# Performance work log

Hardware: AMD Instinct MI355X
Metric: run time of the kernel (lower is better)

Reference implementation:

```python
import jax, jax.numpy as jnp
import numpy as np

N, F_IN, HID, H1, E = 50000, 512, 128, 4, 800000
NEG_SLOPE = 0.2

def setup_inputs() -> dict:
    key = jax.random.key(0)
    ks = jax.random.split(key, 10)
    s = lambda fan: 1.0 / np.sqrt(fan)
    x = jax.random.normal(ks[0], (N, F_IN), jnp.float32)
    edge_index = jax.random.randint(ks[1], (2, E), 0, N, jnp.int32)
    W1 = jax.random.normal(ks[2], (F_IN, H1 * HID), jnp.float32) * s(F_IN)
    a_src1 = jax.random.normal(ks[3], (H1, HID), jnp.float32) * s(HID)
    a_dst1 = jax.random.normal(ks[4], (H1, HID), jnp.float32) * s(HID)
    b1 = jnp.zeros((H1 * HID,), jnp.float32)
    W2 = jax.random.normal(ks[5], (H1 * HID, HID), jnp.float32) * s(H1 * HID)
    a_src2 = jax.random.normal(ks[6], (1, HID), jnp.float32) * s(HID)
    a_dst2 = jax.random.normal(ks[7], (1, HID), jnp.float32) * s(HID)
    b2 = jnp.zeros((HID,), jnp.float32)
    return {"x": x, "edge_index": edge_index, "W1": W1, "a_src1": a_src1,
            "a_dst1": a_dst1, "b1": b1, "W2": W2, "a_src2": a_src2,
            "a_dst2": a_dst2, "b2": b2}

def _gat(x, src, dst, W, a_src, a_dst, b, n):
    H, C = a_src.shape
    h = (x @ W).reshape(-1, H, C)                      # [N, H, C]
    # per-edge attention logits: alpha_src[src] + alpha_dst[dst]
    e = jax.nn.leaky_relu((h * a_src).sum(-1)[src] + (h * a_dst).sum(-1)[dst],
                          NEG_SLOPE)                   # [E', H]
    # segment softmax over destination node
    m = jax.ops.segment_max(e, dst, num_segments=n)
    p = jnp.exp(e - m[dst])
    denom = jax.ops.segment_sum(p, dst, num_segments=n)
    alpha = p / (denom[dst] + 1e-16)
    # weighted scatter-add aggregation
    out = jax.ops.segment_sum(h[src] * alpha[:, :, None], dst, num_segments=n)
    return out.reshape(-1, H * C) + b

def reference(x, edge_index, W1, a_src1, a_dst1, b1, W2, a_src2, a_dst2, b2):
    loops = jnp.arange(N, dtype=edge_index.dtype)      # add_self_loops=True
    src = jnp.concatenate([edge_index[0], loops])
    dst = jnp.concatenate([edge_index[1], loops])
    h = jax.nn.elu(_gat(x, src, dst, W1, a_src1, a_dst1, b1, N))
    return _gat(h, src, dst, W2, a_src2, a_dst2, b2, N)
```

## Files before the change

kernel.cpp:

```cpp
#include <hip/hip_runtime.h>
#include <hip/hip_bf16.h>
#include <math.h>

#define NEG_SLOPE 0.2f

constexpr int N_NODES = 50000;
constexpr int F_IN    = 512;
constexpr int HID     = 128;
constexpr int H1      = 4;
constexpr int E_EDGES = 800000;
constexpr int E_TOT   = E_EDGES + N_NODES;

typedef __attribute__((ext_vector_type(8))) short short8;
typedef __attribute__((ext_vector_type(4))) float floatx4;
typedef __attribute__((ext_vector_type(8))) unsigned short ushort8v;
typedef __attribute__((ext_vector_type(4))) unsigned short ushort4v;
typedef __attribute__((ext_vector_type(2))) unsigned short ushort2v;

__device__ __forceinline__ unsigned short f2bf(float f) {
  union { float f; unsigned int u; } v; v.f = f;
  unsigned int u = v.u + 0x7FFFu + ((v.u >> 16) & 1u);
  return (unsigned short)(u >> 16);
}
__device__ __forceinline__ float bf2f(unsigned short b) {
  union { unsigned int u; float f; } v; v.u = ((unsigned int)b) << 16; return v.f;
}

__device__ __forceinline__ void store_val(float* p, float v) { *p = v; }
__device__ __forceinline__ void store_val(unsigned short* p, float v) { *p = f2bf(v); }

template <int CPT>
__device__ __forceinline__ void load_cvt(const unsigned short* p, float* v) {
  if constexpr (CPT == 8) {
    ushort8v u = *(const ushort8v*)p;
#pragma unroll
    for (int c = 0; c < 8; ++c) v[c] = bf2f(u[c]);
  } else if constexpr (CPT == 4) {
    ushort4v u = *(const ushort4v*)p;
#pragma unroll
    for (int c = 0; c < 4; ++c) v[c] = bf2f(u[c]);
  } else {
    ushort2v u = *(const ushort2v*)p;
#pragma unroll
    for (int c = 0; c < 2; ++c) v[c] = bf2f(u[c]);
  }
}
template <int CPT>
__device__ __forceinline__ void load_cvt(const float* p, float* v) {
#pragma unroll
  for (int c = 0; c < CPT; c += 4) *(float4*)(v + c) = *(const float4*)(p + c);
}

template <int CPT>
__device__ __forceinline__ void store_vec(unsigned short* p, const float* v) {
  if constexpr (CPT == 8) {
    ushort8v o;
#pragma unroll
    for (int c = 0; c < 8; ++c) o[c] = f2bf(v[c]);
    *(ushort8v*)p = o;
  } else if constexpr (CPT == 4) {
    ushort4v o;
#pragma unroll
    for (int c = 0; c < 4; ++c) o[c] = f2bf(v[c]);
    *(ushort4v*)p = o;
  } else {
    ushort2v o;
#pragma unroll
    for (int c = 0; c < 2; ++c) o[c] = f2bf(v[c]);
    *(ushort2v*)p = o;
  }
}
template <int CPT>
__device__ __forceinline__ void store_vec(float* p, const float* v) {
#pragma unroll
  for (int c = 0; c < CPT; c += 4) *(float4*)(p + c) = *(const float4*)(v + c);
}

__device__ __forceinline__ void async_load16(const void* g, void* lds) {
  __builtin_amdgcn_global_load_lds(
      (const __attribute__((address_space(1))) unsigned int*)g,
      (__attribute__((address_space(3))) unsigned int*)lds, 16, 0, 0);
}

__global__ void zero_int_kernel(int* p, int n) {
  int i = blockIdx.x * blockDim.x + threadIdx.x;
  if (i < n) p[i] = 0;
}

__global__ void hist_kernel(const int* __restrict__ ei, int* __restrict__ counts) {
  int i = blockIdx.x * blockDim.x + threadIdx.x;
  if (i < E_EDGES) {
    atomicAdd(&counts[ei[E_EDGES + i]], 1);
  } else if (i < E_TOT) {
    atomicAdd(&counts[i - E_EDGES], 1);
  }
}

__global__ void scan1_kernel(const int* __restrict__ cnt, int* __restrict__ part,
                             int* __restrict__ bsum, int n) {
  __shared__ int buf[256];
  int tid = threadIdx.x, i = blockIdx.x * 256 + tid;
  int v = (i < n) ? cnt[i] : 0;
  buf[tid] = v;
  __syncthreads();
  for (int s = 1; s < 256; s <<= 1) {
    int t = (tid >= s) ? buf[tid - s] : 0;
    __syncthreads();
    buf[tid] += t;
    __syncthreads();
  }
  if (i < n) part[i] = buf[tid] - v;
  if (tid == 255) bsum[blockIdx.x] = buf[255];
}

__global__ void scan2_kernel(int* __restrict__ bsum, int nb) {
  __shared__ int buf[256];
  int tid = threadIdx.x;
  int v = (tid < nb) ? bsum[tid] : 0;
  buf[tid] = v;
  __syncthreads();
  for (int s = 1; s < 256; s <<= 1) {
    int t = (tid >= s) ? buf[tid - s] : 0;
    __syncthreads();
    buf[tid] += t;
    __syncthreads();
  }
  if (tid < nb) bsum[tid] = buf[tid] - v;
  if (tid == 255) bsum[nb] = buf[255];
}

__global__ void scan3_kernel(const int* __restrict__ part, const int* __restrict__ bsum,
                             int* __restrict__ offs, int n) {
  int i = blockIdx.x * 256 + threadIdx.x;
  if (i < n) offs[i] = part[i] + bsum[blockIdx.x];
  if (i == 0) offs[n] = bsum[(n + 255) / 256];
}

__global__ void scatter_kernel(const int* __restrict__ ei, const int* __restrict__ offs,
                               int* __restrict__ cursor, int* __restrict__ sorted_src) {
  int i = blockIdx.x * blockDim.x + threadIdx.x;
  if (i >= E_TOT) return;
  int s, d;
  if (i < E_EDGES) { s = ei[i]; d = ei[E_EDGES + i]; }
  else             { s = i - E_EDGES; d = s; }
  int pos = offs[d] + atomicAdd(&cursor[d], 1);
  sorted_src[pos] = s;
}

__global__ void cast4_kernel(const float* __restrict__ in, unsigned short* __restrict__ out,
                             long n4) {
  long i = (long)blockIdx.x * blockDim.x + threadIdx.x;
  if (i >= n4) return;
  float4 v = ((const float4*)in)[i];
  ushort4 o;
  o.x = f2bf(v.x); o.y = f2bf(v.y); o.z = f2bf(v.z); o.w = f2bf(v.w);
  ((ushort4*)out)[i] = o;
}

__global__ void tcast_kernel(const float* __restrict__ in, unsigned short* __restrict__ out,
                             int K, int N) {
  int idx = blockIdx.x * blockDim.x + threadIdx.x;
  if (idx >= K * N) return;
  int n = idx / K, k = idx - n * K;
  out[idx] = f2bf(in[k * N + n]);
}

template <typename OT>
__global__ __launch_bounds__(256) void gemm_bf16_kernel(
    const unsigned short* __restrict__ A, const unsigned short* __restrict__ Bt,
    OT* __restrict__ C, const float* __restrict__ a_srcp, const float* __restrict__ a_dstp,
    float* __restrict__ alpha_src, float* __restrict__ alpha_dst,
    int M, int N, int K, int Hn) {
  __shared__ unsigned short As[128 * 32];
  __shared__ unsigned short Bs[128 * 32];
  __shared__ float red_s[128][2];
  __shared__ float red_d[128][2];
  int tid = threadIdx.x;
  int lane = tid & 63, wave = tid >> 6;
  int wm = wave & 1, wn = wave >> 1;
  int row0 = blockIdx.x * 128;
  int head = blockIdx.y;
  int col0 = head * 128;
  int l15 = lane & 15, quad = lane >> 4;

  floatx4 acc[4][4];
#pragma unroll
  for (int i = 0; i < 4; ++i)
#pragma unroll
    for (int j = 0; j < 4; ++j) acc[i][j] = (floatx4){0.f, 0.f, 0.f, 0.f};

  int seg_a = wave * 2;
  int r_in = (lane >> 2);
  int c8 = (lane & 3) * 8;

  for (int k0 = 0; k0 < K; k0 += 32) {
#pragma unroll
    for (int p = 0; p < 2; ++p) {
      int seg = seg_a + p;
      int r = seg * 16 + r_in;
      int gr = row0 + r; if (gr >= M) gr = M - 1;
      async_load16(A + (size_t)gr * K + k0 + c8, &As[seg * 512]);
      int gc = col0 + r;
      async_load16(Bt + (size_t)gc * K + k0 + c8, &Bs[seg * 512]);
    }
    __syncthreads();

    short8 a[4], b[4];
#pragma unroll
    for (int mi = 0; mi < 4; ++mi)
      a[mi] = *(const short8*)&As[(wm * 64 + mi * 16 + l15) * 32 + quad * 8];
#pragma unroll
    for (int ni = 0; ni < 4; ++ni)
      b[ni] = *(const short8*)&Bs[(wn * 64 + ni * 16 + l15) * 32 + quad * 8];
#pragma unroll
    for (int mi = 0; mi < 4; ++mi)
#pragma unroll
      for (int ni = 0; ni < 4; ++ni)
        acc[mi][ni] = __builtin_amdgcn_mfma_f32_16x16x32_bf16(a[mi], b[ni], acc[mi][ni], 0, 0, 0);
    __syncthreads();
  }

  float a_s[4], a_d[4];
#pragma unroll
  for (int ni = 0; ni < 4; ++ni) {
    int cih = wn * 64 + ni * 16 + l15;
    a_s[ni] = a_srcp[head * HID + cih];
    a_d[ni] = a_dstp[head * HID + cih];
  }

#pragma unroll
  for (int mi = 0; mi < 4; ++mi) {
#pragma unroll
    for (int r = 0; r < 4; ++r) {
      int rloc = wm * 64 + mi * 16 + quad * 4 + r;
      int grow = row0 + rloc;
      float ps = 0.f, pd = 0.f;
#pragma unroll
      for (int ni = 0; ni < 4; ++ni) {
        float v = acc[mi][ni][r];
        ps += v * a_s[ni];
        pd += v * a_d[ni];
        if (grow < M) {
          int gcol = col0 + wn * 64 + ni * 16 + l15;
          store_val(&C[(size_t)grow * N + gcol], v);
        }
      }
#pragma unroll
      for (int off = 1; off < 16; off <<= 1) {
        ps += __shfl_xor(ps, off);
        pd += __shfl_xor(pd, off);
      }
      if (l15 == 0) { red_s[rloc][wn] = ps; red_d[rloc][wn] = pd; }
    }
  }
  __syncthreads();
  if (tid < 128) {
    int grow = row0 + tid;
    if (grow < M) {
      alpha_src[(size_t)grow * Hn + head] = red_s[tid][0] + red_s[tid][1];
      alpha_dst[(size_t)grow * Hn + head] = red_d[tid][0] + red_d[tid][1];
    }
  }
}

template <int H, int CPT, typename GT, typename OT>
__global__ __launch_bounds__(64) void aggregate_kernel(
    const GT* __restrict__ h, const float* __restrict__ asrc,
    const float* __restrict__ adst, const int* __restrict__ offs,
    const int* __restrict__ sorted_src, const float* __restrict__ bias,
    OT* __restrict__ out, int apply_elu) {
  constexpr int CH = H * HID;
  constexpr int NCH = CH / CPT;
  constexpr int SLOTS = 64 / NCH;
  __shared__ float p_sh[64 * H];
  __shared__ int src_sh[64];
  int node = blockIdx.x;
  int lane = threadIdx.x;
  int off = offs[node];
  int deg = offs[node + 1] - off;
  if (deg > 64) deg = 64;

  int s_i = 0;
  if (lane < deg) s_i = sorted_src[off + lane];
  src_sh[lane] = s_i;

  float ar[H];
#pragma unroll
  for (int hh = 0; hh < H; ++hh) ar[hh] = (lane < deg) ? asrc[s_i * H + hh] : 0.f;
#pragma unroll
  for (int hh = 0; hh < H; ++hh) {
    float v = ar[hh] + adst[node * H + hh];
    v = (v > 0.f) ? v : NEG_SLOPE * v;
    float lg = (lane < deg) ? v : -1e30f;
#pragma unroll
    for (int o = 32; o; o >>= 1) lg = fmaxf(lg, __shfl_xor(lg, o));
    float p = (lane < deg) ? expf(v - lg) : 0.f;
    float s = p;
#pragma unroll
    for (int o = 32; o; o >>= 1) s += __shfl_xor(s, o);
    p_sh[lane * H + hh] = p * (1.f / (s + 1e-16f));
  }
  __syncthreads();

  int chlane = lane % NCH;
  int slot = lane / NCH;
  int ch = chlane * CPT;
  constexpr int HEAD_SHIFT = 7;
  int head = ch >> HEAD_SHIFT;

  float acc[CPT];
#pragma unroll
  for (int c = 0; c < CPT; ++c) acc[c] = 0.f;

  auto body = [&](int e) {
    float w = p_sh[e * H + head];
    const GT* pp = h + (size_t)src_sh[e] * CH + ch;
    float vv[CPT];
    load_cvt<CPT>(pp, vv);
#pragma unroll
    for (int c = 0; c < CPT; ++c) acc[c] += vv[c] * w;
  };
  int e = slot;
  for (; e + 3 * SLOTS < deg; e += 4 * SLOTS) {
    body(e); body(e + SLOTS); body(e + 2 * SLOTS); body(e + 3 * SLOTS);
  }
  for (; e < deg; e += SLOTS) body(e);

  if constexpr (SLOTS == 2) {
#pragma unroll
    for (int c = 0; c < CPT; ++c) acc[c] += __shfl_xor(acc[c], 32);
  }
  if (slot == 0) {
    float r[CPT];
#pragma unroll
    for (int c = 0; c < CPT; ++c) {
      float t = acc[c] + bias[ch + c];
      if (apply_elu) t = (t > 0.f) ? t : (expf(t) - 1.f);
      r[c] = t;
    }
    store_vec<CPT>(&out[(size_t)node * CH + ch], r);
  }
}

extern "C" void kernel_launch(void* const* d_in, const int* in_sizes, int n_in,
                              void* d_out, int out_size, void* d_ws, size_t ws_size,
                              hipStream_t stream) {
  const float* x      = (const float*)d_in[0];
  const int*   ei     = (const int*)d_in[1];
  const float* W1     = (const float*)d_in[2];
  const float* a_src1 = (const float*)d_in[3];
  const float* a_dst1 = (const float*)d_in[4];
  const float* b1     = (const float*)d_in[5];
  const float* W2     = (const float*)d_in[6];
  const float* a_src2 = (const float*)d_in[7];
  const float* a_dst2 = (const float*)d_in[8];
  const float* b2     = (const float*)d_in[9];
  float* out = (float*)d_out;

  float* ws   = (float*)d_ws;
  float* as1  = ws;
  float* ad1  = as1 + N_NODES * H1;
  float* as2  = ad1 + N_NODES * H1;
  float* ad2  = as2 + N_NODES;
  unsigned short* xb    = (unsigned short*)(ad2 + N_NODES);
  unsigned short* h1b   = xb + (size_t)N_NODES * 512;
  unsigned short* hmidb = h1b + (size_t)N_NODES * 512;
  unsigned short* h2b   = hmidb + (size_t)N_NODES * 512;
  unsigned short* W1t   = h2b + (size_t)N_NODES * 128;
  unsigned short* W2t   = W1t + 512 * 512;
  int* counts = (int*)(W2t + 128 * 512);
  int* cursor = counts + N_NODES;
  int* offs   = cursor + N_NODES;
  int* ssrc   = offs + N_NODES + 1;
  int* part   = ssrc + E_TOT;
  int* bsum   = part + N_NODES;

  constexpr int NB = (N_NODES + 255) / 256;

  zero_int_kernel<<<(2 * N_NODES + 255) / 256, 256, 0, stream>>>(counts, 2 * N_NODES);
  hist_kernel<<<(E_TOT + 255) / 256, 256, 0, stream>>>(ei, counts);
  scan1_kernel<<<NB, 256, 0, stream>>>(counts, part, bsum, N_NODES);
  scan2_kernel<<<1, 256, 0, stream>>>(bsum, NB);
  scan3_kernel<<<NB, 256, 0, stream>>>(part, bsum, offs, N_NODES);
  scatter_kernel<<<(E_TOT + 255) / 256, 256, 0, stream>>>(ei, offs, cursor, ssrc);

  long n4x = (long)N_NODES * 512 / 4;
  cast4_kernel<<<(int)((n4x + 255) / 256), 256, 0, stream>>>(x, xb, n4x);
  tcast_kernel<<<(512 * 512 + 255) / 256, 256, 0, stream>>>(W1, W1t, 512, 512);
  tcast_kernel<<<(512 * 128 + 255) / 256, 256, 0, stream>>>(W2, W2t, 512, 128);

  dim3 g1((N_NODES + 127) / 128, 4);
  gemm_bf16_kernel<unsigned short><<<g1, 256, 0, stream>>>(
      xb, W1t, h1b, a_src1, a_dst1, as1, ad1, N_NODES, 512, 512, H1);
  aggregate_kernel<4, 8, unsigned short, unsigned short><<<N_NODES, 64, 0, stream>>>(
      h1b, as1, ad1, offs, ssrc, b1, hmidb, 1);

  dim3 g2((N_NODES + 127) / 128, 1);
  gemm_bf16_kernel<unsigned short><<<g2, 256, 0, stream>>>(
      hmidb, W2t, h2b, a_src2, a_dst2, as2, ad2, N_NODES, 128, 512, 1);
  aggregate_kernel<1, 4, unsigned short, float><<<N_NODES, 64, 0, stream>>>(
      h2b, as2, ad2, offs, ssrc, b2, out, 0);
}
```

Baseline: 515.8 us.

## Fuse x bf16 cast into GEMM, swizzle GEMM blocks, widen aggregate loads

Removes the separate fp32-to-bf16 cast pass over x by converting A tiles inside the first GEMM with synchronous loads. GEMM blocks are remapped so the heads of a group of eight row tiles run adjacently, for L2 reuse of A. The aggregate kernel now always reads 8 bf16 values per lane via uint4, unrolls by eight, and precomputes row offsets. The second layer uses fewer lanes per edge, so more edges are in flight. Also folds the cursor zeroing into scan3 and reuses workspace buffers. The fused cast gives up the async LDS copy for A in layer one, which may stall the GEMM.

Result: no change. 508.5 us (-1.4%).

```diff
diff --git a/kernel.cpp b/kernel.cpp
--- a/kernel.cpp
+++ b/kernel.cpp
@@ -13,61 +13,31 @@
 
 typedef __attribute__((ext_vector_type(8))) short short8;
 typedef __attribute__((ext_vector_type(4))) float floatx4;
-typedef __attribute__((ext_vector_type(8))) unsigned short ushort8v;
 typedef __attribute__((ext_vector_type(4))) unsigned short ushort4v;
-typedef __attribute__((ext_vector_type(2))) unsigned short ushort2v;
 
 __device__ __forceinline__ unsigned short f2bf(float f) {
   union { float f; unsigned int u; } v; v.f = f;
   unsigned int u = v.u + 0x7FFFu + ((v.u >> 16) & 1u);
   return (unsigned short)(u >> 16);
 }
-__device__ __forceinline__ float bf2f(unsigned short b) {
-  union { unsigned int u; float f; } v; v.u = ((unsigned int)b) << 16; return v.f;
+__device__ __forceinline__ float bf_lo(unsigned int u) {
+  union { unsigned int u; float f; } v; v.u = u << 16; return v.f;
+}
+__device__ __forceinline__ float bf_hi(unsigned int u) {
+  union { unsigned int u; float f; } v; v.u = u & 0xFFFF0000u; return v.f;
 }
 
 __device__ __forceinline__ void store_val(float* p, float v) { *p = v; }
 __device__ __forceinline__ void store_val(unsigned short* p, float v) { *p = f2bf(v); }
 
 template <int CPT>
-__device__ __forceinline__ void load_cvt(const unsigned short* p, float* v) {
-  if constexpr (CPT == 8) {
-    ushort8v u = *(const ushort8v*)p;
-#pragma unroll
-    for (int c = 0; c < 8; ++c) v[c] = bf2f(u[c]);
-  } else if constexpr (CPT == 4) {
-    ushort4v u = *(const ushort4v*)p;
-#pragma unroll
-    for (int c = 0; c < 4; ++c) v[c] = bf2f(u[c]);
-  } else {
-    ushort2v u = *(const ushort2v*)p;
-#pragma unroll
-    for (int c = 0; c < 2; ++c) v[c] = bf2f(u[c]);
-  }
-}
-template <int CPT>
-__device__ __forceinline__ void load_cvt(const float* p, float* v) {
-#pragma unroll
-  for (int c = 0; c < CPT; c += 4) *(float4*)(v + c) = *(const float4*)(p + c);
-}
-
-template <int CPT>
 __device__ __forceinline__ void store_vec(unsigned short* p, const float* v) {
-  if constexpr (CPT == 8) {
-    ushort8v o;
-#pragma unroll
-    for (int c = 0; c < 8; ++c) o[c] = f2bf(v[c]);
-    *(ushort8v*)p = o;
-  } else if constexpr (CPT == 4) {
+#pragma unroll
+  for (int c = 0; c < CPT; c += 4) {
     ushort4v o;
 #pragma unroll
-    for (int c = 0; c < 4; ++c) o[c] = f2bf(v[c]);
-    *(ushort4v*)p = o;
-  } else {
-    ushort2v o;
-#pragma unroll
-    for (int c = 0; c < 2; ++c) o[c] = f2bf(v[c]);
-    *(ushort2v*)p = o;
+    for (int j = 0; j < 4; ++j) o[j] = f2bf(v[c + j]);
+    *(ushort4v*)(p + c) = o;
   }
 }
 template <int CPT>
@@ -130,9 +100,9 @@
 }
 
 __global__ void scan3_kernel(const int* __restrict__ part, const int* __restrict__ bsum,
-                             int* __restrict__ offs, int n) {
+                             int* __restrict__ offs, int* __restrict__ cursor, int n) {
   int i = blockIdx.x * 256 + threadIdx.x;
-  if (i < n) offs[i] = part[i] + bsum[blockIdx.x];
+  if (i < n) { offs[i] = part[i] + bsum[blockIdx.x]; cursor[i] = 0; }
   if (i == 0) offs[n] = bsum[(n + 255) / 256];
 }
 
@@ -147,16 +117,6 @@
   sorted_src[pos] = s;
 }
 
-__global__ void cast4_kernel(const float* __restrict__ in, unsigned short* __restrict__ out,
-                             long n4) {
-  long i = (long)blockIdx.x * blockDim.x + threadIdx.x;
-  if (i >= n4) return;
-  float4 v = ((const float4*)in)[i];
-  ushort4 o;
-  o.x = f2bf(v.x); o.y = f2bf(v.y); o.z = f2bf(v.z); o.w = f2bf(v.w);
-  ((ushort4*)out)[i] = o;
-}
-
 __global__ void tcast_kernel(const float* __restrict__ in, unsigned short* __restrict__ out,
                              int K, int N) {
   int idx = blockIdx.x * blockDim.x + threadIdx.x;
@@ -165,22 +125,28 @@
   out[idx] = f2bf(in[k * N + n]);
 }
 
-template <typename OT>
+template <bool CVT_A, typename OT>
 __global__ __launch_bounds__(256) void gemm_bf16_kernel(
-    const unsigned short* __restrict__ A, const unsigned short* __restrict__ Bt,
+    const void* __restrict__ Araw, const unsigned short* __restrict__ Bt,
     OT* __restrict__ C, const float* __restrict__ a_srcp, const float* __restrict__ a_dstp,
     float* __restrict__ alpha_src, float* __restrict__ alpha_dst,
-    int M, int N, int K, int Hn) {
+    int M, int N, int K, int Hn, int nRowTiles) {
   __shared__ unsigned short As[128 * 32];
   __shared__ unsigned short Bs[128 * 32];
   __shared__ float red_s[128][2];
   __shared__ float red_d[128][2];
+
+  int grp = blockIdx.x / (8 * Hn);
+  int w8 = blockIdx.x % (8 * Hn);
+  int head = w8 >> 3;
+  int rowTile = grp * 8 + (w8 & 7);
+  if (rowTile >= nRowTiles) return;
+  int row0 = rowTile * 128;
+  int col0 = head * 128;
+
   int tid = threadIdx.x;
   int lane = tid & 63, wave = tid >> 6;
   int wm = wave & 1, wn = wave >> 1;
-  int row0 = blockIdx.x * 128;
-  int head = blockIdx.y;
-  int col0 = head * 128;
   int l15 = lane & 15, quad = lane >> 4;
 
   floatx4 acc[4][4];
@@ -189,19 +155,40 @@
 #pragma unroll
     for (int j = 0; j < 4; ++j) acc[i][j] = (floatx4){0.f, 0.f, 0.f, 0.f};
 
-  int seg_a = wave * 2;
+  int seg_b = wave * 2;
   int r_in = (lane >> 2);
   int c8 = (lane & 3) * 8;
 
   for (int k0 = 0; k0 < K; k0 += 32) {
 #pragma unroll
     for (int p = 0; p < 2; ++p) {
-      int seg = seg_a + p;
+      int seg = seg_b + p;
       int r = seg * 16 + r_in;
-      int gr = row0 + r; if (gr >= M) gr = M - 1;
-      async_load16(A + (size_t)gr * K + k0 + c8, &As[seg * 512]);
       int gc = col0 + r;
       async_load16(Bt + (size_t)gc * K + k0 + c8, &Bs[seg * 512]);
+    }
+    if constexpr (CVT_A) {
+      const float* Af = (const float*)Araw;
+#pragma unroll
+      for (int p = 0; p < 4; ++p) {
+        int lin = tid + p * 256;
+        int r = lin >> 3;
+        int q = lin & 7;
+        int gr = row0 + r; if (gr >= M) gr = M - 1;
+        float4 f = *(const float4*)(Af + (size_t)gr * K + k0 + q * 4);
+        ushort4v o;
+        o[0] = f2bf(f.x); o[1] = f2bf(f.y); o[2] = f2bf(f.z); o[3] = f2bf(f.w);
+        *(ushort4v*)&As[r * 32 + q * 4] = o;
+      }
+    } else {
+      const unsigned short* Ab = (const unsigned short*)Araw;
+#pragma unroll
+      for (int p = 0; p < 2; ++p) {
+        int seg = seg_b + p;
+        int r = seg * 16 + r_in;
+        int gr = row0 + r; if (gr >= M) gr = M - 1;
+        async_load16(Ab + (size_t)gr * K + k0 + c8, &As[seg * 512]);
+      }
     }
     __syncthreads();
 
@@ -263,17 +250,18 @@
   }
 }
 
-template <int H, int CPT, typename GT, typename OT>
+template <int H, typename OT>
 __global__ __launch_bounds__(64) void aggregate_kernel(
-    const GT* __restrict__ h, const float* __restrict__ asrc,
+    const unsigned short* __restrict__ h, const float* __restrict__ asrc,
     const float* __restrict__ adst, const int* __restrict__ offs,
     const int* __restrict__ sorted_src, const float* __restrict__ bias,
     OT* __restrict__ out, int apply_elu) {
+  constexpr int CPT = 8;
   constexpr int CH = H * HID;
   constexpr int NCH = CH / CPT;
   constexpr int SLOTS = 64 / NCH;
   __shared__ float p_sh[64 * H];
-  __shared__ int src_sh[64];
+  __shared__ int rowoff_sh[64];
   int node = blockIdx.x;
   int lane = threadIdx.x;
   int off = offs[node];
@@ -282,7 +270,7 @@
 
   int s_i = 0;
   if (lane < deg) s_i = sorted_src[off + lane];
-  src_sh[lane] = s_i;
+  rowoff_sh[lane] = s_i * CH;
 
   float ar[H];
 #pragma unroll
@@ -305,8 +293,7 @@
   int chlane = lane % NCH;
   int slot = lane / NCH;
   int ch = chlane * CPT;
-  constexpr int HEAD_SHIFT = 7;
-  int head = ch >> HEAD_SHIFT;
+  int head = ch >> 7;
 
   float acc[CPT];
 #pragma unroll
@@ -314,22 +301,25 @@
 
   auto body = [&](int e) {
     float w = p_sh[e * H + head];
-    const GT* pp = h + (size_t)src_sh[e] * CH + ch;
-    float vv[CPT];
-    load_cvt<CPT>(pp, vv);
-#pragma unroll
-    for (int c = 0; c < CPT; ++c) acc[c] += vv[c] * w;
+    uint4 u = *(const uint4*)(h + (size_t)(unsigned)rowoff_sh[e] + ch);
+    acc[0] += bf_lo(u.x) * w;  acc[1] += bf_hi(u.x) * w;
+    acc[2] += bf_lo(u.y) * w;  acc[3] += bf_hi(u.y) * w;
+    acc[4] += bf_lo(u.z) * w;  acc[5] += bf_hi(u.z) * w;
+    acc[6] += bf_lo(u.w) * w;  acc[7] += bf_hi(u.w) * w;
   };
   int e = slot;
-  for (; e + 3 * SLOTS < deg; e += 4 * SLOTS) {
+  for (; e + 7 * SLOTS < deg; e += 8 * SLOTS) {
     body(e); body(e + SLOTS); body(e + 2 * SLOTS); body(e + 3 * SLOTS);
-  }
+    body(e + 4 * SLOTS); body(e + 5 * SLOTS); body(e + 6 * SLOTS); body(e + 7 * SLOTS);
+  }
+  for (; e + SLOTS < deg; e += 2 * SLOTS) { body(e); body(e + SLOTS); }
   for (; e < deg; e += SLOTS) body(e);
 
-  if constexpr (SLOTS == 2) {
-#pragma unroll
-    for (int c = 0; c < CPT; ++c) acc[c] += __shfl_xor(acc[c], 32);
-  }
+#pragma unroll
+  for (int o = NCH; o < 64; o <<= 1)
+#pragma unroll
+    for (int c = 0; c < CPT; ++c) acc[c] += __shfl_xor(acc[c], o);
+
   if (slot == 0) {
     float r[CPT];
 #pragma unroll
@@ -362,11 +352,12 @@
   float* ad1  = as1 + N_NODES * H1;
   float* as2  = ad1 + N_NODES * H1;
   float* ad2  = as2 + N_NODES;
-  unsigned short* xb    = (unsigned short*)(ad2 + N_NODES);
-  unsigned short* h1b   = xb + (size_t)N_NODES * 512;
-  unsigned short* hmidb = h1b + (size_t)N_NODES * 512;
-  unsigned short* h2b   = hmidb + (size_t)N_NODES * 512;
-  unsigned short* W1t   = h2b + (size_t)N_NODES * 128;
+  unsigned short* bufA = (unsigned short*)(ad2 + N_NODES);
+  unsigned short* bufB = bufA + (size_t)N_NODES * 512;
+  unsigned short* hmidb = bufA;
+  unsigned short* h1b   = bufB;
+  unsigned short* h2b   = bufB;
+  unsigned short* W1t   = bufB + (size_t)N_NODES * 512;
   unsigned short* W2t   = W1t + 512 * 512;
   int* counts = (int*)(W2t + 128 * 512);
   int* cursor = counts + N_NODES;
@@ -376,28 +367,26 @@
   int* bsum   = part + N_NODES;
 
   constexpr int NB = (N_NODES + 255) / 256;
-
-  zero_int_kernel<<<(2 * N_NODES + 255) / 256, 256, 0, stream>>>(counts, 2 * N_NODES);
+  constexpr int NRT = (N_NODES + 127) / 128;
+  constexpr int NRT8 = ((NRT + 7) / 8) * 8;
+
+  zero_int_kernel<<<(N_NODES + 255) / 256, 256, 0, stream>>>(counts, N_NODES);
   hist_kernel<<<(E_TOT + 255) / 256, 256, 0, stream>>>(ei, counts);
   scan1_kernel<<<NB, 256, 0, stream>>>(counts, part, bsum, N_NODES);
   scan2_kernel<<<1, 256, 0, stream>>>(bsum, NB);
-  scan3_kernel<<<NB, 256, 0, stream>>>(part, bsum, offs, N_NODES);
+  scan3_kernel<<<NB, 256, 0, stream>>>(part, bsum, offs, cursor, N_NODES);
   scatter_kernel<<<(E_TOT + 255) / 256, 256, 0, stream>>>(ei, offs, cursor, ssrc);
 
-  long n4x = (long)N_NODES * 512 / 4;
-  cast4_kernel<<<(int)((n4x + 255) / 256), 256, 0, stream>>>(x, xb, n4x);
   tcast_kernel<<<(512 * 512 + 255) / 256, 256, 0, stream>>>(W1, W1t, 512, 512);
   tcast_kernel<<<(512 * 128 + 255) / 256, 256, 0, stream>>>(W2, W2t, 512, 128);
 
-  dim3 g1((N_NODES + 127) / 128, 4);
-  gemm_bf16_kernel<unsigned short><<<g1, 256, 0, stream>>>(
-      xb, W1t, h1b, a_src1, a_dst1, as1, ad1, N_NODES, 512, 512, H1);
-  aggregate_kernel<4, 8, unsigned short, unsigned short><<<N_NODES, 64, 0, stream>>>(
+  gemm_bf16_kernel<true, unsigned short><<<NRT8 * H1, 256, 0, stream>>>(
+      x, W1t, h1b, a_src1, a_dst1, as1, ad1, N_NODES, 512, 512, H1, NRT);
+  aggregate_kernel<4, unsigned short><<<N_NODES, 64, 0, stream>>>(
       h1b, as1, ad1, offs, ssrc, b1, hmidb, 1);
 
-  dim3 g2((N_NODES + 127) / 128, 1);
-  gemm_bf16_kernel<unsigned short><<<g2, 256, 0, stream>>>(
-      hmidb, W2t, h2b, a_src2, a_dst2, as2, ad2, N_NODES, 128, 512, 1);
-  aggregate_kernel<1, 4, unsigned short, float><<<N_NODES, 64, 0, stream>>>(
+  gemm_bf16_kernel<false, unsigned short><<<NRT8, 256, 0, stream>>>(
+      hmidb, W2t, h2b, a_src2, a_dst2, as2, ad2, N_NODES, 128, 512, 1, NRT);
+  aggregate_kernel<1, float><<<N_NODES, 64, 0, stream>>>(
       h2b, as2, ad2, offs, ssrc, b2, out, 0);
 }
```
